# Kernel optimization log

Hardware: AMD Instinct MI355X
Metric: run time of the kernel (lower is better)

Reference implementation:

```python
import jax, jax.numpy as jnp
import numpy as np
import math

EPS = 1e-5  # torch BatchNorm2d default eps
EXPANSION_RATE = 2


def _bn_train(x, gamma, beta):
    # BatchNorm2d in training mode: biased batch statistics over (B, H, W)
    mu = jnp.mean(x, axis=(0, 2, 3), keepdims=True)
    var = jnp.var(x, axis=(0, 2, 3), keepdims=True)
    xn = (x - mu) * jax.lax.rsqrt(var + EPS)
    return gamma[None, :, None, None] * xn + beta[None, :, None, None]


def _conv1x1(x, w, b):
    # w: [O, C]  (1x1 conv kernel squeezed), b: [O]
    return jnp.einsum('bchw,oc->bohw', x, w) + b[None, :, None, None]


def _lsgc(x, w_diff, b_diff, g_bn, be_bn, w_in, b_in, g_ibn, be_ibn,
          w_mr, b_mr, g_mbn, be_mbn):
    B, C, H, W = x.shape
    bit_depth = max(math.ceil(math.log2(H)), math.ceil(math.log2(W)))
    steps = [EXPANSION_RATE * 2 ** (n - 1) for n in range(1, bit_depth + 1)]

    fmax = None
    for step in steps:
        for axis, size in ((3, W), (2, H)):
            s = step % size
            for sgn in (1, -1):  # forward / backward rolls
                shifted = jnp.roll(x, sgn * s, axis=axis) if s else x
                d = x - shifted
                fmax = d if fmax is None else jnp.maximum(fmax, d)

    x_diff = _bn_train(_conv1x1(fmax, w_diff, b_diff), g_bn, be_bn)
    x_proc = _bn_train(_conv1x1(x, w_in, b_in), g_ibn, be_ibn)

    # MRConv: concat -> 1x1 conv -> BN -> GELU (exact) -> residual add
    x_cat = jnp.concatenate([x_proc, x_diff], axis=1)
    h = _bn_train(_conv1x1(x_cat, w_mr, b_mr), g_mbn, be_mbn)
    h = jax.nn.gelu(h, approximate=False)
    return x_proc + h


def setup_inputs() -> dict:
    key = jax.random.key(0)
    ks = jax.random.split(key, 8)
    B, C_in, C_out, H, W = 32, 128, 128, 64, 64

    def kaiming(k, o, i):
        return jax.random.normal(k, (o, i), jnp.float32) * np.sqrt(2.0 / i)

    return {
        'x': jax.random.normal(ks[0], (B, C_in, H, W), jnp.float32),
        'w_diff': kaiming(ks[1], C_out, C_in),
        'b_diff': jnp.zeros((C_out,), jnp.float32),
        'g_bn': jnp.ones((C_out,), jnp.float32),
        'be_bn': jnp.zeros((C_out,), jnp.float32),
        'w_in': kaiming(ks[2], C_out, C_in),
        'b_in': jnp.zeros((C_out,), jnp.float32),
        'g_ibn': jnp.ones((C_out,), jnp.float32),
        'be_ibn': jnp.zeros((C_out,), jnp.float32),
        'w_mr': kaiming(ks[3], C_out, 2 * C_out),
        'b_mr': jnp.zeros((C_out,), jnp.float32),
        'g_mbn': jnp.ones((C_out,), jnp.float32),
        'be_mbn': jnp.zeros((C_out,), jnp.float32),
    }


def reference(x, w_diff, b_diff, g_bn, be_bn, w_in, b_in, g_ibn, be_ibn,
              w_mr, b_mr, g_mbn, be_mbn):
    return _lsgc(x, w_diff, b_diff, g_bn, be_bn, w_in, b_in, g_ibn, be_ibn,
                 w_mr, b_mr, g_mbn, be_mbn)
```

## Files before the change

kernel.cpp:

```cpp
#include <hip/hip_runtime.h>
#include <math.h>


#define INV_NPIX (1.0f / 131072.0f)
#define EPS 1e-5f
#define T1 4
#define T2 2

typedef __attribute__((ext_vector_type(8))) short s16x8;
typedef __attribute__((ext_vector_type(4))) float f32x4;

__device__ __forceinline__ uint32_t bf16_rne(float v) {
  uint32_t x = __float_as_uint(v);
  return (x + 0x7fffu + ((x >> 16) & 1u)) >> 16;
}
__device__ __forceinline__ uint32_t pack_hl(float v) {
  uint32_t h = bf16_rne(v);
  float lo = v - __uint_as_float(h << 16);
  return h | (bf16_rne(lo) << 16);
}
__device__ __forceinline__ float bf_lo(uint32_t d) {
  return __uint_as_float(d << 16);
}
__device__ __forceinline__ float bf_hi(uint32_t d) {
  return __uint_as_float(d & 0xffff0000u);
}
__device__ __forceinline__ float4 fmin4(float4 a, float4 b) {
  return make_float4(fminf(a.x, b.x), fminf(a.y, b.y), fminf(a.z, b.z),
                     fminf(a.w, b.w));
}

__global__ __launch_bounds__(256) void stencil_prep_kernel(
    const float* __restrict__ x, uint32_t* __restrict__ xp,
    uint32_t* __restrict__ fp, const float* __restrict__ w_in,
    const float* __restrict__ w_diff, unsigned short* __restrict__ wInH,
    unsigned short* __restrict__ wInL, unsigned short* __restrict__ wDfH,
    unsigned short* __restrict__ wDfL) {
  __shared__ float4 pA[1024];
  __shared__ float4 pB[1024];
  if (blockIdx.x >= 2048) {
    const int t = (blockIdx.x - 2048) * 256 + threadIdx.x;
    const int e = t & 16383;
    const float* w = (t < 16384) ? w_in : w_diff;
    unsigned short* aH = (t < 16384) ? wInH : wDfH;
    unsigned short* aL = (t < 16384) ? wInL : wDfL;
    const int j = e & 7, l = (e >> 3) & 63, mt = (e >> 9) & 7, kc = e >> 12;
    const int m = mt * 16 + (l & 15);
    const int k = kc * 32 + ((l >> 4) << 3) + j;
    const uint32_t p = pack_hl(w[m * 128 + k]);
    aH[e] = (unsigned short)(p & 0xffffu);
    aL[e] = (unsigned short)(p >> 16);
    return;
  }
  const int b = blockIdx.x >> 6;
  const int cp = blockIdx.x & 63;
  const float4* xa = (const float4*)x + (size_t)(b * 128 + 2 * cp) * 1024;
  const float4* xb = xa + 1024;
  float4 sA[4], sB[4];
#pragma unroll
  for (int i = 0; i < 4; ++i) {
    const int u = threadIdx.x + i * 256;
    sA[i] = xa[u];
    sB[i] = xb[u];
    pA[u] = sA[i];
    pB[u] = sB[i];
  }
  __syncthreads();
  const size_t obase = (size_t)(b * 64 + cp) * 1024;
#pragma unroll
  for (int i = 0; i < 4; ++i) {
    const int u = threadIdx.x + i * 256;
    const int h = u >> 4, wu = u & 15;
    const int row = u & ~15;
    float4 mA, mB;
    {
      const float4 A = sA[i];
      const float4 L = pA[row | ((wu + 15) & 15)];
      const float4 R = pA[row | ((wu + 1) & 15)];
      float4 m = fmin4(A, fmin4(L, R));
      m = fmin4(m, make_float4(A.z, A.w, R.x, R.y));
      m = fmin4(m, make_float4(L.z, L.w, A.x, A.y));
      m = fmin4(m, pA[row | ((wu + 2) & 15)]);
      m = fmin4(m, pA[row | ((wu + 14) & 15)]);
      m = fmin4(m, pA[row | ((wu + 4) & 15)]);
      m = fmin4(m, pA[row | ((wu + 12) & 15)]);
      m = fmin4(m, pA[row | ((wu + 8) & 15)]);
      m = fmin4(m, pA[(((h + 2) & 63) << 4) | wu]);
      m = fmin4(m, pA[(((h + 62) & 63) << 4) | wu]);
      m = fmin4(m, pA[(((h + 4) & 63) << 4) | wu]);
      m = fmin4(m, pA[(((h + 60) & 63) << 4) | wu]);
      m = fmin4(m, pA[(((h + 8) & 63) << 4) | wu]);
      m = fmin4(m, pA[(((h + 56) & 63) << 4) | wu]);
      m = fmin4(m, pA[(((h + 16) & 63) << 4) | wu]);
      m = fmin4(m, pA[(((h + 48) & 63) << 4) | wu]);
      m = fmin4(m, pA[(((h + 32) & 63) << 4) | wu]);
      mA = m;
    }
    {
      const float4 A = sB[i];
      const float4 L = pB[row | ((wu + 15) & 15)];
      const float4 R = pB[row | ((wu + 1) & 15)];
      float4 m = fmin4(A, fmin4(L, R));
      m = fmin4(m, make_float4(A.z, A.w, R.x, R.y));
      m = fmin4(m, make_float4(L.z, L.w, A.x, A.y));
      m = fmin4(m, pB[row | ((wu + 2) & 15)]);
      m = fmin4(m, pB[row | ((wu + 14) & 15)]);
      m = fmin4(m, pB[row | ((wu + 4) & 15)]);
      m = fmin4(m, pB[row | ((wu + 12) & 15)]);
      m = fmin4(m, pB[row | ((wu + 8) & 15)]);
      m = fmin4(m, pB[(((h + 2) & 63) << 4) | wu]);
      m = fmin4(m, pB[(((h + 62) & 63) << 4) | wu]);
      m = fmin4(m, pB[(((h + 4) & 63) << 4) | wu]);
      m = fmin4(m, pB[(((h + 60) & 63) << 4) | wu]);
      m = fmin4(m, pB[(((h + 8) & 63) << 4) | wu]);
      m = fmin4(m, pB[(((h + 56) & 63) << 4) | wu]);
      m = fmin4(m, pB[(((h + 16) & 63) << 4) | wu]);
      m = fmin4(m, pB[(((h + 48) & 63) << 4) | wu]);
      m = fmin4(m, pB[(((h + 32) & 63) << 4) | wu]);
      mB = m;
    }
    uint4 px, pf;
    px.x = bf16_rne(sA[i].x) | (bf16_rne(sB[i].x) << 16);
    px.y = bf16_rne(sA[i].y) | (bf16_rne(sB[i].y) << 16);
    px.z = bf16_rne(sA[i].z) | (bf16_rne(sB[i].z) << 16);
    px.w = bf16_rne(sA[i].w) | (bf16_rne(sB[i].w) << 16);
    pf.x = bf16_rne(sA[i].x - mA.x) | (bf16_rne(sB[i].x - mB.x) << 16);
    pf.y = bf16_rne(sA[i].y - mA.y) | (bf16_rne(sB[i].y - mB.y) << 16);
    pf.z = bf16_rne(sA[i].z - mA.z) | (bf16_rne(sB[i].z - mB.z) << 16);
    pf.w = bf16_rne(sA[i].w - mA.w) | (bf16_rne(sB[i].w - mB.w) << 16);
    ((uint4*)xp)[obase + u] = px;
    ((uint4*)fp)[obase + u] = pf;
  }
}

__device__ __forceinline__ void stage_tile(const uint32_t* __restrict__ B,
                                           const int b, const int hw0,
                                           uint32_t* lbuf, const int wave,
                                           const int lane) {
  const int qq = lane >> 4, ln = lane & 15;
#pragma unroll
  for (int i = 0; i < 4; ++i) {
    const int row = wave * 16 + i * 4 + qq;
    const uint32_t* src =
        &B[((size_t)(b * 64 + row)) * 4096 + hw0 + ((ln * 4) ^ (i << 4))];
    uint32_t* dst = lbuf + (wave * 16 + i * 4) * 64;
    __builtin_amdgcn_global_load_lds(
        (const __attribute__((address_space(1))) void*)src,
        (__attribute__((address_space(3))) void*)dst, 16, 0, 0);
  }
}

__device__ __forceinline__ void cwrite_stats(
    const f32x4 (&acc)[2][4], uint32_t* __restrict__ outp,
    float* __restrict__ pS, float* __restrict__ pQ, const int bx,
    const int wave, const int q, const int ln) {
  const int b = bx >> 6, hw0 = (bx & 63) << 6;
#pragma unroll
  for (int mt2 = 0; mt2 < 2; ++mt2) {
    float sa[4] = {0.f, 0.f, 0.f, 0.f};
    float sq[4] = {0.f, 0.f, 0.f, 0.f};
#pragma unroll
    for (int nt = 0; nt < 4; ++nt) {
#pragma unroll
      for (int rp = 0; rp < 2; ++rp) {
        const float v0 = acc[mt2][nt][2 * rp];
        const float v1 = acc[mt2][nt][2 * rp + 1];
        const int m2 = (wave * 2 + mt2) * 8 + q * 2 + rp;
        outp[((size_t)(b * 64 + m2)) * 4096 + hw0 + nt * 16 + ln] =
            bf16_rne(v0) | (bf16_rne(v1) << 16);
        sa[2 * rp] += v0;
        sq[2 * rp] += v0 * v0;
        sa[2 * rp + 1] += v1;
        sq[2 * rp + 1] += v1 * v1;
      }
    }
#pragma unroll
    for (int off = 1; off < 16; off <<= 1) {
#pragma unroll
      for (int r = 0; r < 4; ++r) {
        sa[r] += __shfl_xor(sa[r], off);
        sq[r] += __shfl_xor(sq[r], off);
      }
    }
    if (ln == 0) {
#pragma unroll
      for (int r = 0; r < 4; ++r) {
        const int m = (wave * 2 + mt2) * 16 + q * 4 + r;
        pS[bx * 128 + m] = sa[r];
        pQ[bx * 128 + m] = sq[r];
      }
    }
  }
}

template <int T>
__device__ __forceinline__ void gemm1_persist(
    const unsigned short* __restrict__ AH, const unsigned short* __restrict__ AL,
    const uint32_t* __restrict__ B0, uint32_t* __restrict__ outp,
    float* __restrict__ pS, float* __restrict__ pQ, const int p,
    uint32_t* Bs) {
  const int tid = threadIdx.x;
  const int lane = tid & 63;
  const int wave = tid >> 6;
  const int q = lane >> 4;
  const int ln = lane & 15;

  stage_tile(B0, (p * T) >> 6, ((p * T) & 63) << 6, Bs, wave, lane);

  f32x4 accA[2][4], accB[2][4];

#pragma unroll
  for (int t = 0; t < T; ++t) {
    const int bx = p * T + t;
    uint32_t* buf = Bs + (t & 1) * 4096;
    __syncthreads();
    if (t + 1 < T) {
      const int bn = bx + 1;
      stage_tile(B0, bn >> 6, (bn & 63) << 6, Bs + ((t + 1) & 1) * 4096, wave,
                 lane);
    }
    s16x8 ah[2][2], al[2][2];
#pragma unroll
    for (int mt2 = 0; mt2 < 2; ++mt2) {
      const size_t off = ((size_t)((wave * 2 + mt2) * 64 + lane)) << 3;
      ah[0][mt2] = *(const s16x8*)(AH + off);
      al[0][mt2] = *(const s16x8*)(AL + off);
    }
    if (t > 0)
      cwrite_stats((t & 1) ? accA : accB, outp, pS, pQ, bx - 1, wave, q, ln);
    f32x4(&acc)[2][4] = (t & 1) ? accB : accA;
#pragma unroll
    for (int i = 0; i < 2; ++i)
#pragma unroll
      for (int jj = 0; jj < 4; ++jj) acc[i][jj] = (f32x4)(0.0f);
#pragma unroll
    for (int kc = 0; kc < 4; ++kc) {
      if (kc < 3) {
#pragma unroll
        for (int mt2 = 0; mt2 < 2; ++mt2) {
          const size_t off =
              ((size_t)(((kc + 1) * 8 + wave * 2 + mt2) * 64 + lane)) << 3;
          ah[(kc + 1) & 1][mt2] = *(const s16x8*)(AH + off);
          al[(kc + 1) & 1][mt2] = *(const s16x8*)(AL + off);
        }
      }
#pragma unroll
      for (int nt = 0; nt < 4; ++nt) {
        union { uint32_t u[4]; s16x8 s; } bb;
#pragma unroll
        for (int j = 0; j < 4; ++j)
          bb.u[j] =
              buf[(kc * 16 + q * 4 + j) * 64 + ((nt * 16 + ln) ^ (q << 4))];
#pragma unroll
        for (int mt2 = 0; mt2 < 2; ++mt2) {
          acc[mt2][nt] = __builtin_amdgcn_mfma_f32_16x16x32_bf16(
              ah[kc & 1][mt2], bb.s, acc[mt2][nt], 0, 0, 0);
          acc[mt2][nt] = __builtin_amdgcn_mfma_f32_16x16x32_bf16(
              al[kc & 1][mt2], bb.s, acc[mt2][nt], 0, 0, 0);
        }
      }
    }
  }
  cwrite_stats(((T - 1) & 1) ? accB : accA, outp, pS, pQ, p * T + T - 1, wave,
               q, ln);
}

__global__ __launch_bounds__(256) void gemm1_dual(
    const unsigned short* __restrict__ AH1, const unsigned short* __restrict__ AL1,
    const uint32_t* __restrict__ XP, uint32_t* __restrict__ out1,
    float* __restrict__ sv1, float* __restrict__ sq1,
    const unsigned short* __restrict__ AH2, const unsigned short* __restrict__ AL2,
    const uint32_t* __restrict__ FP, uint32_t* __restrict__ out2,
    float* __restrict__ sv2, float* __restrict__ sq2) {
  __shared__ uint32_t Bs[2 * 4096];
  const int p = blockIdx.x & 511;
  if (blockIdx.x < 512)
    gemm1_persist<T1>(AH1, AL1, XP, out1, sv1, sq1, p, Bs);
  else
    gemm1_persist<T1>(AH2, AL2, FP, out2, sv2, sq2, p, Bs);
}

template <int T>
__device__ __forceinline__ void gemm2_persist(
    const unsigned short* __restrict__ AH, const unsigned short* __restrict__ AL,
    const uint32_t* __restrict__ B0, const uint32_t* __restrict__ B1,
    uint32_t* __restrict__ outp, float* __restrict__ pS,
    float* __restrict__ pQ, const int p, uint32_t* Bs) {
  const int tid = threadIdx.x;
  const int lane = tid & 63;
  const int wave = tid >> 6;
  const int q = lane >> 4;
  const int ln = lane & 15;

  stage_tile(B0, (p * T) >> 6, ((p * T) & 63) << 6, Bs, wave, lane);

  f32x4 accA[2][4], accB[2][4];

#pragma unroll
  for (int s = 0; s < 2 * T; ++s) {
    const int t = s >> 1, half = s & 1;
    const int bx = p * T + t;
    uint32_t* buf = Bs + (s & 1) * 4096;
    __syncthreads();
    if (s + 1 < 2 * T) {
      const int s2 = s + 1;
      const int bx2 = p * T + (s2 >> 1);
      stage_tile((s2 & 1) ? B1 : B0, bx2 >> 6, (bx2 & 63) << 6,
                 Bs + (s2 & 1) * 4096, wave, lane);
    }
    const int kb = half * 4;
    s16x8 ah[2][2], al[2][2];
#pragma unroll
    for (int mt2 = 0; mt2 < 2; ++mt2) {
      const size_t off =
          ((size_t)((kb * 8 + wave * 2 + mt2) * 64 + lane)) << 3;
      ah[0][mt2] = *(const s16x8*)(AH + off);
      al[0][mt2] = *(const s16x8*)(AL + off);
    }
    f32x4(&acc)[2][4] = (t & 1) ? accB : accA;
    if (half == 0) {
      if (t > 0)
        cwrite_stats((t & 1) ? accA : accB, outp, pS, pQ, bx - 1, wave, q, ln);
#pragma unroll
      for (int i = 0; i < 2; ++i)
#pragma unroll
        for (int jj = 0; jj < 4; ++jj) acc[i][jj] = (f32x4)(0.0f);
    }
#pragma unroll
    for (int kc = 0; kc < 4; ++kc) {
      if (kc < 3) {
#pragma unroll
        for (int mt2 = 0; mt2 < 2; ++mt2) {
          const size_t off =
              ((size_t)(((kb + kc + 1) * 8 + wave * 2 + mt2) * 64 + lane))
              << 3;
          ah[(kc + 1) & 1][mt2] = *(const s16x8*)(AH + off);
          al[(kc + 1) & 1][mt2] = *(const s16x8*)(AL + off);
        }
      }
#pragma unroll
      for (int nt = 0; nt < 4; ++nt) {
        union { uint32_t u[4]; s16x8 s; } bb;
#pragma unroll
        for (int j = 0; j < 4; ++j)
          bb.u[j] =
              buf[(kc * 16 + q * 4 + j) * 64 + ((nt * 16 + ln) ^ (q << 4))];
#pragma unroll
        for (int mt2 = 0; mt2 < 2; ++mt2) {
          acc[mt2][nt] = __builtin_amdgcn_mfma_f32_16x16x32_bf16(
              ah[kc & 1][mt2], bb.s, acc[mt2][nt], 0, 0, 0);
          acc[mt2][nt] = __builtin_amdgcn_mfma_f32_16x16x32_bf16(
              al[kc & 1][mt2], bb.s, acc[mt2][nt], 0, 0, 0);
        }
      }
    }
  }
  cwrite_stats(((T - 1) & 1) ? accB : accA, outp, pS, pQ, p * T + T - 1, wave,
               q, ln);
}

__global__ __launch_bounds__(256) void gemm2_kernel(
    const unsigned short* __restrict__ AH, const unsigned short* __restrict__ AL,
    const uint32_t* __restrict__ B0, const uint32_t* __restrict__ B1,
    uint32_t* __restrict__ outp, float* __restrict__ sv,
    float* __restrict__ sq) {
  __shared__ uint32_t Bs[2 * 4096];
  gemm2_persist<T2>(AH, AL, B0, B1, outp, sv, sq, blockIdx.x, Bs);
}

__global__ __launch_bounds__(256) void reduce_kernel(
    const float* __restrict__ P, float* __restrict__ p2) {
  const int a = blockIdx.x >> 4, g = blockIdx.x & 15;
  const int c = threadIdx.x & 127, h = threadIdx.x >> 7;
  const float* src = P + ((size_t)(a * 2048 + g * 128 + h * 64)) * 128 + c;
  float s0 = 0.f, s1 = 0.f, s2 = 0.f, s3 = 0.f;
#pragma unroll
  for (int j = 0; j < 64; j += 4) {
    s0 += src[(j + 0) * 128];
    s1 += src[(j + 1) * 128];
    s2 += src[(j + 2) * 128];
    s3 += src[(j + 3) * 128];
  }
  __shared__ float sm[256];
  sm[threadIdx.x] = (s0 + s1) + (s2 + s3);
  __syncthreads();
  if (h == 0) p2[(a * 16 + g) * 128 + c] = sm[c] + sm[128 + c];
}

__global__ __launch_bounds__(256) void finalize1_kernel(
    const float* __restrict__ p2, const float* __restrict__ g_ibn,
    const float* __restrict__ be_ibn, const float* __restrict__ g_bn,
    const float* __restrict__ w_mr, float* __restrict__ a_in,
    float* __restrict__ d_in, unsigned short* __restrict__ wEffH,
    unsigned short* __restrict__ wEffL) {
  __shared__ float sa[256];
  const int t = threadIdx.x;
  if (t < 128) {
    float s = 0.f, qq = 0.f;
#pragma unroll
    for (int g = 0; g < 16; ++g) {
      s += p2[g * 128 + t];
      qq += p2[(16 + g) * 128 + t];
    }
    const float mu = s * INV_NPIX;
    const float var = fmaxf(qq * INV_NPIX - mu * mu, 0.f);
    const float a = g_ibn[t] * rsqrtf(var + EPS);
    if (blockIdx.x == 0) {
      a_in[t] = a;
      d_in[t] = be_ibn[t] - mu * a;
    }
    sa[t] = a;
  } else {
    const int c = t - 128;
    float s = 0.f, qq = 0.f;
#pragma unroll
    for (int g = 0; g < 16; ++g) {
      s += p2[(32 + g) * 128 + c];
      qq += p2[(48 + g) * 128 + c];
    }
    const float mu = s * INV_NPIX;
    const float var = fmaxf(qq * INV_NPIX - mu * mu, 0.f);
    sa[t] = g_bn[c] * rsqrtf(var + EPS);
  }
  __syncthreads();
  const int e = blockIdx.x * 256 + t;
  const int j = e & 7, l = (e >> 3) & 63, mt = (e >> 9) & 7, kc = e >> 12;
  const int m = mt * 16 + (l & 15);
  const int k = kc * 32 + ((l >> 4) << 3) + j;
  const uint32_t p = pack_hl(w_mr[m * 256 + k] * sa[k]);
  wEffH[e] = (unsigned short)(p & 0xffffu);
  wEffL[e] = (unsigned short)(p >> 16);
}

__device__ __forceinline__ float gelu_exact(float z) {
  return 0.5f * z * (1.0f + erff(z * 0.70710678118654752f));
}

__global__ __launch_bounds__(256) void epilogue_kernel(
    const uint32_t* __restrict__ yp, const uint32_t* __restrict__ hp,
    const float* __restrict__ a_in, const float* __restrict__ d_in,
    const float* __restrict__ p2h, const float* __restrict__ g_mbn,
    const float* __restrict__ be_mbn, float* __restrict__ out) {
  __shared__ float sAi[128], sDi[128], sAm[128], sDm[128];
  const int tid = threadIdx.x;
  if (tid < 128) {
    float s = 0.f, qq = 0.f;
#pragma unroll
    for (int g = 0; g < 16; ++g) {
      s += p2h[g * 128 + tid];
      qq += p2h[(16 + g) * 128 + tid];
    }
    const float mu = s * INV_NPIX;
    const float var = fmaxf(qq * INV_NPIX - mu * mu, 0.f);
    const float a = g_mbn[tid] * rsqrtf(var + EPS);
    sAm[tid] = a;
    sDm[tid] = be_mbn[tid] - mu * a;
    sAi[tid] = a_in[tid];
    sDi[tid] = d_in[tid];
  }
  __syncthreads();
#pragma unroll
  for (int it = 0; it < 4; ++it) {
    const size_t i = (size_t)(blockIdx.x * 4 + it) * 256 + tid;
    const int cp = (int)((i >> 10) & 63);
    const int b = (int)(i >> 16);
    const int c0 = 2 * cp, c1 = 2 * cp + 1;
    const uint4 yv = ((const uint4*)yp)[i];
    const uint4 hv = ((const uint4*)hp)[i];
    const float a0 = sAi[c0], d0 = sDi[c0], m0 = sAm[c0], e0 = sDm[c0];
    const float a1 = sAi[c1], d1 = sDi[c1], m1 = sAm[c1], e1 = sDm[c1];
    float4 o0, o1;
    o0.x = fmaf(a0, bf_lo(yv.x), d0) + gelu_exact(fmaf(m0, bf_lo(hv.x), e0));
    o0.y = fmaf(a0, bf_lo(yv.y), d0) + gelu_exact(fmaf(m0, bf_lo(hv.y), e0));
    o0.z = fmaf(a0, bf_lo(yv.z), d0) + gelu_exact(fmaf(m0, bf_lo(hv.z), e0));
    o0.w = fmaf(a0, bf_lo(yv.w), d0) + gelu_exact(fmaf(m0, bf_lo(hv.w), e0));
    o1.x = fmaf(a1, bf_hi(yv.x), d1) + gelu_exact(fmaf(m1, bf_hi(hv.x), e1));
    o1.y = fmaf(a1, bf_hi(yv.y), d1) + gelu_exact(fmaf(m1, bf_hi(hv.y), e1));
    o1.z = fmaf(a1, bf_hi(yv.z), d1) + gelu_exact(fmaf(m1, bf_hi(hv.z), e1));
    o1.w = fmaf(a1, bf_hi(yv.w), d1) + gelu_exact(fmaf(m1, bf_hi(hv.w), e1));
    const size_t u = i & 1023;
    ((float4*)out)[(size_t)(b * 128 + c0) * 1024 + u] = o0;
    ((float4*)out)[(size_t)(b * 128 + c1) * 1024 + u] = o1;
  }
}

extern "C" void kernel_launch(void* const* d_in, const int* in_sizes, int n_in,
                              void* d_out, int out_size, void* d_ws,
                              size_t ws_size, hipStream_t stream) {
  const float* x = (const float*)d_in[0];
  const float* w_diff = (const float*)d_in[1];
  const float* g_bn = (const float*)d_in[3];
  const float* w_in = (const float*)d_in[5];
  const float* g_ibn = (const float*)d_in[7];
  const float* be_ibn = (const float*)d_in[8];
  const float* w_mr = (const float*)d_in[9];
  const float* g_mbn = (const float*)d_in[11];
  const float* be_mbn = (const float*)d_in[12];
  float* out = (float*)d_out;

  const size_t PD = (size_t)8388608;
  uint32_t* ws = (uint32_t*)d_ws;
  uint32_t* xp = ws;
  uint32_t* fpx = ws + PD;
  uint32_t* ypIn = ws + 2 * PD;
  uint32_t* ypDf = ws + 3 * PD;
  uint32_t* hp = ws + 4 * PD;
  float* st = (float*)(ws + 5 * PD);
  float* p2 = st;
  float* p2h = st + 8192;
  float* a_in = st + 12288, *dinc = st + 12416;
  unsigned short* fr = (unsigned short*)(st + 12800);
  unsigned short* wInH = fr;
  unsigned short* wInL = fr + 16384;
  unsigned short* wDfH = fr + 32768;
  unsigned short* wDfL = fr + 49152;
  unsigned short* wEffH = fr + 65536;
  unsigned short* wEffL = fr + 98304;
  float* g1p = (float*)(ws + 4 * PD);
  float* g2p = (float*)ws;

  stencil_prep_kernel<<<2176, 256, 0, stream>>>(x, xp, fpx, w_in, w_diff,
                                                wInH, wInL, wDfH, wDfL);
  gemm1_dual<<<1024, 256, 0, stream>>>(wInH, wInL, xp, ypIn, g1p,
                                       g1p + 262144, wDfH, wDfL, fpx, ypDf,
                                       g1p + 524288, g1p + 786432);
  reduce_kernel<<<64, 256, 0, stream>>>(g1p, p2);
  finalize1_kernel<<<128, 256, 0, stream>>>(p2, g_ibn, be_ibn, g_bn, w_mr,
                                            a_in, dinc, wEffH, wEffL);
  gemm2_kernel<<<1024, 256, 0, stream>>>(wEffH, wEffL, ypIn, ypDf, hp, g2p,
                                         g2p + 262144);
  reduce_kernel<<<32, 256, 0, stream>>>(g2p, p2h);
  epilogue_kernel<<<2048, 256, 0, stream>>>(ypIn, hp, a_in, dinc, p2h, g_mbn,
                                            be_mbn, out);
}
```

Baseline: 241.8 us.

## Tile-major intermediate layout and XOR-swizzled LDS stencil buffer

Changes the bf16 intermediate buffers from channel-pair-major planes to a per-(batch, 64-pixel tile) contiguous layout, so each GEMM tile stage reads one contiguous 16KB block and the output writes are contiguous. The stencil prep kernel now writes scattered 256B chunks per row, and the final epilogue reads with a matching remap. It also XOR-swizzles the stencil's LDS float4 array by row to reduce bank conflicts on vertical-neighbour reads. The trade is less coalescing on the prep writes and the epilogue reads.

New measurement: 244.2 us. No clear change (+1.0%).

```diff
diff --git a/kernel.cpp b/kernel.cpp
--- a/kernel.cpp
+++ b/kernel.cpp
@@ -29,6 +29,8 @@
   return make_float4(fminf(a.x, b.x), fminf(a.y, b.y), fminf(a.z, b.z),
                      fminf(a.w, b.w));
 }
+
+#define RD(P, hh, ww) P[(((hh) & 63) << 4) | (((ww) & 15) ^ ((hh) & 7))]
 
 __global__ __launch_bounds__(256) void stencil_prep_kernel(
     const float* __restrict__ x, uint32_t* __restrict__ xp,
@@ -60,63 +62,62 @@
 #pragma unroll
   for (int i = 0; i < 4; ++i) {
     const int u = threadIdx.x + i * 256;
+    const int h = u >> 4, wu = u & 15;
     sA[i] = xa[u];
     sB[i] = xb[u];
-    pA[u] = sA[i];
-    pB[u] = sB[i];
+    RD(pA, h, wu) = sA[i];
+    RD(pB, h, wu) = sB[i];
   }
   __syncthreads();
-  const size_t obase = (size_t)(b * 64 + cp) * 1024;
 #pragma unroll
   for (int i = 0; i < 4; ++i) {
     const int u = threadIdx.x + i * 256;
     const int h = u >> 4, wu = u & 15;
-    const int row = u & ~15;
     float4 mA, mB;
     {
       const float4 A = sA[i];
-      const float4 L = pA[row | ((wu + 15) & 15)];
-      const float4 R = pA[row | ((wu + 1) & 15)];
+      const float4 L = RD(pA, h, wu + 15);
+      const float4 R = RD(pA, h, wu + 1);
       float4 m = fmin4(A, fmin4(L, R));
       m = fmin4(m, make_float4(A.z, A.w, R.x, R.y));
       m = fmin4(m, make_float4(L.z, L.w, A.x, A.y));
-      m = fmin4(m, pA[row | ((wu + 2) & 15)]);
-      m = fmin4(m, pA[row | ((wu + 14) & 15)]);
-      m = fmin4(m, pA[row | ((wu + 4) & 15)]);
-      m = fmin4(m, pA[row | ((wu + 12) & 15)]);
-      m = fmin4(m, pA[row | ((wu + 8) & 15)]);
-      m = fmin4(m, pA[(((h + 2) & 63) << 4) | wu]);
-      m = fmin4(m, pA[(((h + 62) & 63) << 4) | wu]);
-      m = fmin4(m, pA[(((h + 4) & 63) << 4) | wu]);
-      m = fmin4(m, pA[(((h + 60) & 63) << 4) | wu]);
-      m = fmin4(m, pA[(((h + 8) & 63) << 4) | wu]);
-      m = fmin4(m, pA[(((h + 56) & 63) << 4) | wu]);
-      m = fmin4(m, pA[(((h + 16) & 63) << 4) | wu]);
-      m = fmin4(m, pA[(((h + 48) & 63) << 4) | wu]);
-      m = fmin4(m, pA[(((h + 32) & 63) << 4) | wu]);
+      m = fmin4(m, RD(pA, h, wu + 2));
+      m = fmin4(m, RD(pA, h, wu + 14));
+      m = fmin4(m, RD(pA, h, wu + 4));
+      m = fmin4(m, RD(pA, h, wu + 12));
+      m = fmin4(m, RD(pA, h, wu + 8));
+      m = fmin4(m, RD(pA, h + 2, wu));
+      m = fmin4(m, RD(pA, h + 62, wu));
+      m = fmin4(m, RD(pA, h + 4, wu));
+      m = fmin4(m, RD(pA, h + 60, wu));
+      m = fmin4(m, RD(pA, h + 8, wu));
+      m = fmin4(m, RD(pA, h + 56, wu));
+      m = fmin4(m, RD(pA, h + 16, wu));
+      m = fmin4(m, RD(pA, h + 48, wu));
+      m = fmin4(m, RD(pA, h + 32, wu));
       mA = m;
     }
     {
       const float4 A = sB[i];
-      const float4 L = pB[row | ((wu + 15) & 15)];
-      const float4 R = pB[row | ((wu + 1) & 15)];
+      const float4 L = RD(pB, h, wu + 15);
+      const float4 R = RD(pB, h, wu + 1);
       float4 m = fmin4(A, fmin4(L, R));
       m = fmin4(m, make_float4(A.z, A.w, R.x, R.y));
       m = fmin4(m, make_float4(L.z, L.w, A.x, A.y));
-      m = fmin4(m, pB[row | ((wu + 2) & 15)]);
-      m = fmin4(m, pB[row | ((wu + 14) & 15)]);
-      m = fmin4(m, pB[row | ((wu + 4) & 15)]);
-      m = fmin4(m, pB[row | ((wu + 12) & 15)]);
-      m = fmin4(m, pB[row | ((wu + 8) & 15)]);
-      m = fmin4(m, pB[(((h + 2) & 63) << 4) | wu]);
-      m = fmin4(m, pB[(((h + 62) & 63) << 4) | wu]);
-      m = fmin4(m, pB[(((h + 4) & 63) << 4) | wu]);
-      m = fmin4(m, pB[(((h + 60) & 63) << 4) | wu]);
-      m = fmin4(m, pB[(((h + 8) & 63) << 4) | wu]);
-      m = fmin4(m, pB[(((h + 56) & 63) << 4) | wu]);
-      m = fmin4(m, pB[(((h + 16) & 63) << 4) | wu]);
-      m = fmin4(m, pB[(((h + 48) & 63) << 4) | wu]);
-      m = fmin4(m, pB[(((h + 32) & 63) << 4) | wu]);
+      m = fmin4(m, RD(pB, h, wu + 2));
+      m = fmin4(m, RD(pB, h, wu + 14));
+      m = fmin4(m, RD(pB, h, wu + 4));
+      m = fmin4(m, RD(pB, h, wu + 12));
+      m = fmin4(m, RD(pB, h, wu + 8));
+      m = fmin4(m, RD(pB, h + 2, wu));
+      m = fmin4(m, RD(pB, h + 62, wu));
+      m = fmin4(m, RD(pB, h + 4, wu));
+      m = fmin4(m, RD(pB, h + 60, wu));
+      m = fmin4(m, RD(pB, h + 8, wu));
+      m = fmin4(m, RD(pB, h + 56, wu));
+      m = fmin4(m, RD(pB, h + 16, wu));
+      m = fmin4(m, RD(pB, h + 48, wu));
+      m = fmin4(m, RD(pB, h + 32, wu));
       mB = m;
     }
     uint4 px, pf;
@@ -128,21 +129,20 @@
     pf.y = bf16_rne(sA[i].y - mA.y) | (bf16_rne(sB[i].y - mB.y) << 16);
     pf.z = bf16_rne(sA[i].z - mA.z) | (bf16_rne(sB[i].z - mB.z) << 16);
     pf.w = bf16_rne(sA[i].w - mA.w) | (bf16_rne(sB[i].w - mB.w) << 16);
-    ((uint4*)xp)[obase + u] = px;
-    ((uint4*)fp)[obase + u] = pf;
+    const size_t o = (size_t)(b * 64 + (u >> 4)) * 1024 + cp * 16 + (u & 15);
+    ((uint4*)xp)[o] = px;
+    ((uint4*)fp)[o] = pf;
   }
 }
 
 __device__ __forceinline__ void stage_tile(const uint32_t* __restrict__ B,
-                                           const int b, const int hw0,
-                                           uint32_t* lbuf, const int wave,
-                                           const int lane) {
+                                           const int bx, uint32_t* lbuf,
+                                           const int wave, const int lane) {
   const int qq = lane >> 4, ln = lane & 15;
 #pragma unroll
   for (int i = 0; i < 4; ++i) {
     const int row = wave * 16 + i * 4 + qq;
-    const uint32_t* src =
-        &B[((size_t)(b * 64 + row)) * 4096 + hw0 + ((ln * 4) ^ (i << 4))];
+    const uint32_t* src = &B[(size_t)bx * 4096 + row * 64 + ((ln * 4) ^ (i << 4))];
     uint32_t* dst = lbuf + (wave * 16 + i * 4) * 64;
     __builtin_amdgcn_global_load_lds(
         (const __attribute__((address_space(1))) void*)src,
@@ -154,7 +154,6 @@
     const f32x4 (&acc)[2][4], uint32_t* __restrict__ outp,
     float* __restrict__ pS, float* __restrict__ pQ, const int bx,
     const int wave, const int q, const int ln) {
-  const int b = bx >> 6, hw0 = (bx & 63) << 6;
 #pragma unroll
   for (int mt2 = 0; mt2 < 2; ++mt2) {
     float sa[4] = {0.f, 0.f, 0.f, 0.f};
@@ -166,7 +165,7 @@
         const float v0 = acc[mt2][nt][2 * rp];
         const float v1 = acc[mt2][nt][2 * rp + 1];
         const int m2 = (wave * 2 + mt2) * 8 + q * 2 + rp;
-        outp[((size_t)(b * 64 + m2)) * 4096 + hw0 + nt * 16 + ln] =
+        outp[(size_t)bx * 4096 + m2 * 64 + nt * 16 + ln] =
             bf16_rne(v0) | (bf16_rne(v1) << 16);
         sa[2 * rp] += v0;
         sq[2 * rp] += v0 * v0;
@@ -205,7 +204,7 @@
   const int q = lane >> 4;
   const int ln = lane & 15;
 
-  stage_tile(B0, (p * T) >> 6, ((p * T) & 63) << 6, Bs, wave, lane);
+  stage_tile(B0, p * T, Bs, wave, lane);
 
   f32x4 accA[2][4], accB[2][4];
 
@@ -214,11 +213,7 @@
     const int bx = p * T + t;
     uint32_t* buf = Bs + (t & 1) * 4096;
     __syncthreads();
-    if (t + 1 < T) {
-      const int bn = bx + 1;
-      stage_tile(B0, bn >> 6, (bn & 63) << 6, Bs + ((t + 1) & 1) * 4096, wave,
-                 lane);
-    }
+    if (t + 1 < T) stage_tile(B0, bx + 1, Bs + ((t + 1) & 1) * 4096, wave, lane);
     s16x8 ah[2][2], al[2][2];
 #pragma unroll
     for (int mt2 = 0; mt2 < 2; ++mt2) {
@@ -292,7 +287,7 @@
   const int q = lane >> 4;
   const int ln = lane & 15;
 
-  stage_tile(B0, (p * T) >> 6, ((p * T) & 63) << 6, Bs, wave, lane);
+  stage_tile(B0, p * T, Bs, wave, lane);
 
   f32x4 accA[2][4], accB[2][4];
 
@@ -304,16 +299,14 @@
     __syncthreads();
     if (s + 1 < 2 * T) {
       const int s2 = s + 1;
-      const int bx2 = p * T + (s2 >> 1);
-      stage_tile((s2 & 1) ? B1 : B0, bx2 >> 6, (bx2 & 63) << 6,
-                 Bs + (s2 & 1) * 4096, wave, lane);
+      stage_tile((s2 & 1) ? B1 : B0, p * T + (s2 >> 1), Bs + (s2 & 1) * 4096,
+                 wave, lane);
     }
     const int kb = half * 4;
     s16x8 ah[2][2], al[2][2];
 #pragma unroll
     for (int mt2 = 0; mt2 < 2; ++mt2) {
-      const size_t off =
-          ((size_t)((kb * 8 + wave * 2 + mt2) * 64 + lane)) << 3;
+      const size_t off = ((size_t)((kb * 8 + wave * 2 + mt2) * 64 + lane)) << 3;
       ah[0][mt2] = *(const s16x8*)(AH + off);
       al[0][mt2] = *(const s16x8*)(AL + off);
     }
@@ -332,8 +325,7 @@
 #pragma unroll
         for (int mt2 = 0; mt2 < 2; ++mt2) {
           const size_t off =
-              ((size_t)(((kb + kc + 1) * 8 + wave * 2 + mt2) * 64 + lane))
-              << 3;
+              ((size_t)(((kb + kc + 1) * 8 + wave * 2 + mt2) * 64 + lane)) << 3;
           ah[(kc + 1) & 1][mt2] = *(const s16x8*)(AH + off);
           al[(kc + 1) & 1][mt2] = *(const s16x8*)(AL + off);
         }
@@ -464,9 +456,11 @@
     const size_t i = (size_t)(blockIdx.x * 4 + it) * 256 + tid;
     const int cp = (int)((i >> 10) & 63);
     const int b = (int)(i >> 16);
+    const int u = (int)(i & 1023);
     const int c0 = 2 * cp, c1 = 2 * cp + 1;
-    const uint4 yv = ((const uint4*)yp)[i];
-    const uint4 hv = ((const uint4*)hp)[i];
+    const size_t rp4 = (size_t)(b * 64 + (u >> 4)) * 1024 + cp * 16 + (u & 15);
+    const uint4 yv = ((const uint4*)yp)[rp4];
+    const uint4 hv = ((const uint4*)hp)[rp4];
     const float a0 = sAi[c0], d0 = sDi[c0], m0 = sAm[c0], e0 = sDm[c0];
     const float a1 = sAi[c1], d1 = sDi[c1], m1 = sAm[c1], e1 = sDm[c1];
     float4 o0, o1;
@@ -478,7 +472,6 @@
     o1.y = fmaf(a1, bf_hi(yv.y), d1) + gelu_exact(fmaf(m1, bf_hi(hv.y), e1));
     o1.z = fmaf(a1, bf_hi(yv.z), d1) + gelu_exact(fmaf(m1, bf_hi(hv.z), e1));
     o1.w = fmaf(a1, bf_hi(yv.w), d1) + gelu_exact(fmaf(m1, bf_hi(hv.w), e1));
-    const size_t u = i & 1023;
     ((float4*)out)[(size_t)(b * 128 + c0) * 1024 + u] = o0;
     ((float4*)out)[(size_t)(b * 128 + c1) * 1024 + u] = o1;
   }
```
